# Optimization experiments

Hardware: AMD Instinct MI355X
Metric: run time of the kernel (lower is better)

The kernel has to match this reference:

```python
import jax, jax.numpy as jnp
import numpy as np

B, N, ATTR = 8, 16384, 14
G, M = 256, 32
ENC = 1024
DIM, DEPTH, HEADS = 384, 12, 6
HID = 4 * DIM
FETCH = (3, 7, 11)


def setup_inputs() -> dict:
    key = jax.random.key(0)
    ks = iter(jax.random.split(key, 40))
    def rn(shape, s=0.02):
        return jax.random.normal(next(ks), shape, dtype=jnp.float32) * s
    inp = {}
    inp["xyz"] = jax.random.normal(next(ks), (B, N, ATTR), dtype=jnp.float32)
    # T-Net: 6 -> 64 -> 512 -> 36 (6x6 transform)
    inp["tn_c1_w"] = rn((64, 6));    inp["tn_c1_b"] = jnp.zeros((64,), jnp.float32)
    inp["tn_bn1_g"] = jnp.ones((64,), jnp.float32);  inp["tn_bn1_b"] = jnp.zeros((64,), jnp.float32)
    inp["tn_c2_w"] = rn((512, 64));  inp["tn_c2_b"] = jnp.zeros((512,), jnp.float32)
    inp["tn_bn2_g"] = jnp.ones((512,), jnp.float32); inp["tn_bn2_b"] = jnp.zeros((512,), jnp.float32)
    inp["tn_fc_w"] = rn((36, 512));  inp["tn_fc_b"] = jnp.zeros((36,), jnp.float32)
    # PointNet encoder: ATTR -> 128 -> 256 -> 512 -> ENC (1x1 convs)
    for i, (o, c) in enumerate([(128, ATTR), (256, 128), (512, 256), (ENC, 512)], 1):
        inp[f"e_c{i}_w"] = rn((o, c)); inp[f"e_c{i}_b"] = jnp.zeros((o,), jnp.float32)
        inp[f"e_bn{i}_g"] = jnp.ones((o,), jnp.float32); inp[f"e_bn{i}_b"] = jnp.zeros((o,), jnp.float32)
    inp["reduce_w"] = rn((DIM, ENC)); inp["reduce_b"] = jnp.zeros((DIM,), jnp.float32)
    inp["pos1_w"] = rn((128, 3));     inp["pos1_b"] = jnp.zeros((128,), jnp.float32)
    inp["pos2_w"] = rn((DIM, 128));   inp["pos2_b"] = jnp.zeros((DIM,), jnp.float32)
    # transformer blocks, stacked over depth
    inp["ln1_g"] = jnp.ones((DEPTH, DIM), jnp.float32); inp["ln1_b"] = jnp.zeros((DEPTH, DIM), jnp.float32)
    inp["qkv_w"] = rn((DEPTH, 3 * DIM, DIM))
    inp["proj_w"] = rn((DEPTH, DIM, DIM)); inp["proj_b"] = jnp.zeros((DEPTH, DIM), jnp.float32)
    inp["ln2_g"] = jnp.ones((DEPTH, DIM), jnp.float32); inp["ln2_b"] = jnp.zeros((DEPTH, DIM), jnp.float32)
    inp["fc1_w"] = rn((DEPTH, HID, DIM)); inp["fc1_b"] = jnp.zeros((DEPTH, HID), jnp.float32)
    inp["fc2_w"] = rn((DEPTH, DIM, HID)); inp["fc2_b"] = jnp.zeros((DEPTH, DIM), jnp.float32)
    return inp


def _bn(x, g, b, eps=1e-5):
    # training-mode BatchNorm1d over [batch, length, channel]
    m = jnp.mean(x, axis=(0, 1))
    v = jnp.var(x, axis=(0, 1))
    return (x - m) * jax.lax.rsqrt(v + eps) * g + b


def _lnorm(x, g, b, eps=1e-5):
    m = jnp.mean(x, axis=-1, keepdims=True)
    v = jnp.var(x, axis=-1, keepdims=True)
    return (x - m) * jax.lax.rsqrt(v + eps) * g + b


def _fps(xyz, npoint):
    # sequential farthest point sampling (deterministic start at index 0)
    b, n, _ = xyz.shape
    coords = xyz[:, :, :3]
    bidx = jnp.arange(b)
    def step(carry, _):
        dist, far = carry
        c = coords[bidx, far]                                   # [B,3]
        d = jnp.sum((coords - c[:, None, :]) ** 2, axis=-1)     # [B,N]
        dist = jnp.minimum(dist, d)
        return (dist, jnp.argmax(dist, axis=-1)), far
    init = (jnp.full((b, n), 1e10, jnp.float32), jnp.zeros((b,), jnp.int32))
    _, idxs = jax.lax.scan(step, init, None, length=npoint)
    return jnp.transpose(idxs)                                   # [B,npoint]


def _forward(xyz, tn_c1_w, tn_c1_b, tn_bn1_g, tn_bn1_b, tn_c2_w, tn_c2_b, tn_bn2_g, tn_bn2_b,
             tn_fc_w, tn_fc_b,
             e_c1_w, e_c1_b, e_bn1_g, e_bn1_b, e_c2_w, e_c2_b, e_bn2_g, e_bn2_b,
             e_c3_w, e_c3_b, e_bn3_g, e_bn3_b, e_c4_w, e_c4_b, e_bn4_g, e_bn4_b,
             reduce_w, reduce_b, pos1_w, pos1_b, pos2_w, pos2_b,
             ln1_g, ln1_b, qkv_w, proj_w, proj_b, ln2_g, ln2_b,
             fc1_w, fc1_b, fc2_w, fc2_b):
    b = xyz.shape[0]
    # ---- grouping: FPS + attribute-space KNN (cdist over all A attrs) ----
    cidx = _fps(xyz, G)                                          # [B,G]
    cattrs = jnp.take_along_axis(xyz, cidx[:, :, None], axis=1)  # [B,G,A]
    center = cattrs[:, :, :3]                                    # [B,G,3]
    d2 = (jnp.sum(cattrs ** 2, -1)[:, :, None] + jnp.sum(xyz ** 2, -1)[:, None, :]
          - 2.0 * jnp.einsum('bga,bna->bgn', cattrs, xyz))       # [B,G,N]
    _, knn = jax.lax.top_k(-d2, M)                               # [B,G,M] smallest dists
    nb = jnp.take_along_axis(xyz, knn.reshape(b, G * M)[:, :, None], axis=1)
    nb = nb.reshape(b, G, M, ATTR)
    nb = jnp.concatenate([nb[..., :3] - center[:, :, None, :], nb[..., 3:]], axis=-1)
    # ---- PointNet encoder with 6x6 T-Net on the first 6 attributes ----
    pg = nb.reshape(b * G, M, ATTR)
    x6 = pg[:, :, :6]
    h = jax.nn.relu(_bn(jnp.einsum('bmc,oc->bmo', x6, tn_c1_w) + tn_c1_b, tn_bn1_g, tn_bn1_b))
    h = jax.nn.relu(_bn(jnp.einsum('bmc,oc->bmo', h, tn_c2_w) + tn_c2_b, tn_bn2_g, tn_bn2_b))
    h = jnp.max(h, axis=1)                                       # [BG,512]
    t = (h @ tn_fc_w.T + tn_fc_b + jnp.eye(6, dtype=jnp.float32).reshape(36)).reshape(-1, 6, 6)
    pg = jnp.concatenate([jnp.einsum('bmc,bck->bmk', x6, t), pg[:, :, 6:]], axis=-1)
    p = jax.nn.relu(_bn(jnp.einsum('bmc,oc->bmo', pg, e_c1_w) + e_c1_b, e_bn1_g, e_bn1_b))
    p = jax.nn.relu(_bn(jnp.einsum('bmc,oc->bmo', p, e_c2_w) + e_c2_b, e_bn2_g, e_bn2_b))
    p = jax.nn.relu(_bn(jnp.einsum('bmc,oc->bmo', p, e_c3_w) + e_c3_b, e_bn3_g, e_bn3_b))
    p = _bn(jnp.einsum('bmc,oc->bmo', p, e_c4_w) + e_c4_b, e_bn4_g, e_bn4_b)
    tokens = jnp.max(p, axis=1).reshape(b, G, ENC)               # [B,G,ENC]
    # ---- transformer over group tokens, pos added each layer ----
    x = tokens @ reduce_w.T + reduce_b                           # [B,G,DIM]
    pos = jax.nn.gelu(center @ pos1_w.T + pos1_b) @ pos2_w.T + pos2_b
    scale = (DIM // HEADS) ** -0.5
    feats = []
    for i in range(DEPTH):
        h_in = x + pos
        y = _lnorm(h_in, ln1_g[i], ln1_b[i])
        qkv = jnp.einsum('bnc,oc->bno', y, qkv_w[i]).reshape(b, G, 3, HEADS, DIM // HEADS)
        q, k, v = jnp.moveaxis(qkv, 2, 0)                        # each [B,G,H,D]
        a = jax.nn.softmax(jnp.einsum('bnhd,bmhd->bhnm', q, k) * scale, axis=-1)
        o = jnp.einsum('bhnm,bmhd->bnhd', a, v).reshape(b, G, DIM)
        x = h_in + (jnp.einsum('bnc,oc->bno', o, proj_w[i]) + proj_b[i])
        y = _lnorm(x, ln2_g[i], ln2_b[i])
        y = jax.nn.gelu(jnp.einsum('bnc,oc->bno', y, fc1_w[i]) + fc1_b[i])
        x = x + (jnp.einsum('bnc,oc->bno', y, fc2_w[i]) + fc2_b[i])
        if i in FETCH:
            feats.append(x)
    return jnp.stack(feats)                                      # [3,B,G,DIM]


def reference(xyz, tn_c1_w, tn_c1_b, tn_bn1_g, tn_bn1_b, tn_c2_w, tn_c2_b, tn_bn2_g, tn_bn2_b,
              tn_fc_w, tn_fc_b,
              e_c1_w, e_c1_b, e_bn1_g, e_bn1_b, e_c2_w, e_c2_b, e_bn2_g, e_bn2_b,
              e_c3_w, e_c3_b, e_bn3_g, e_bn3_b, e_c4_w, e_c4_b, e_bn4_g, e_bn4_b,
              reduce_w, reduce_b, pos1_w, pos1_b, pos2_w, pos2_b,
              ln1_g, ln1_b, qkv_w, proj_w, proj_b, ln2_g, ln2_b,
              fc1_w, fc1_b, fc2_w, fc2_b):
    return _forward(xyz, tn_c1_w, tn_c1_b, tn_bn1_g, tn_bn1_b, tn_c2_w, tn_c2_b, tn_bn2_g, tn_bn2_b,
                    tn_fc_w, tn_fc_b,
                    e_c1_w, e_c1_b, e_bn1_g, e_bn1_b, e_c2_w, e_c2_b, e_bn2_g, e_bn2_b,
                    e_c3_w, e_c3_b, e_bn3_g, e_bn3_b, e_c4_w, e_c4_b, e_bn4_g, e_bn4_b,
                    reduce_w, reduce_b, pos1_w, pos1_b, pos2_w, pos2_b,
                    ln1_g, ln1_b, qkv_w, proj_w, proj_b, ln2_g, ln2_b,
                    fc1_w, fc1_b, fc2_w, fc2_b)
```

## Files before the change

kernel.cpp:

```cpp
#include <hip/hip_runtime.h>
#include <hip/hip_bf16.h>
#include <math.h>

typedef __hip_bfloat16 bf16;
typedef __attribute__((ext_vector_type(8))) short bfrag;
typedef __attribute__((ext_vector_type(4))) float f32x4;

constexpr int B_ = 8, N_ = 16384, ATTR_ = 14, G_ = 256, M_ = 32;
constexpr int BG = B_ * G_;
constexpr int ROWS = BG * M_;
constexpr int DIM_ = 384, HEADS_ = 6;

static inline int cdiv(int a, int b) { return (a + b - 1) / b; }

__device__ __forceinline__ float gelu_f(float x) {
  float x3 = x * x * x;
  float t = tanhf(0.7978845608028654f * (x + 0.044715f * x3));
  return 0.5f * x * (1.0f + t);
}

__global__ __launch_bounds__(1024) void fps_kernel(const float* __restrict__ xyz,
                                                   int* __restrict__ cidx) {
  const int b = blockIdx.x;
  const int tid = threadIdx.x;
  const float* base = xyz + (size_t)b * N_ * ATTR_;
  float px[16], py[16], pz[16], dist[16];
#pragma unroll
  for (int j = 0; j < 16; ++j) {
    int n = tid + j * 1024;
    px[j] = base[(size_t)n * ATTR_ + 0];
    py[j] = base[(size_t)n * ATTR_ + 1];
    pz[j] = base[(size_t)n * ATTR_ + 2];
    dist[j] = 1e10f;
  }
  __shared__ float s_v[16];
  __shared__ int s_i[16];
  __shared__ float s_cx, s_cy, s_cz;
  int far = 0;
  float cx = base[0], cy = base[1], cz = base[2];
  for (int g = 0; g < G_; ++g) {
    if (tid == 0) cidx[b * G_ + g] = far;
    float best = -1.0f; int bi = 0;
#pragma unroll
    for (int j = 0; j < 16; ++j) {
      float dx = __fsub_rn(px[j], cx);
      float dy = __fsub_rn(py[j], cy);
      float dz = __fsub_rn(pz[j], cz);
      float d = __fadd_rn(__fadd_rn(__fmul_rn(dx, dx), __fmul_rn(dy, dy)), __fmul_rn(dz, dz));
      float nd = fminf(dist[j], d);
      dist[j] = nd;
      int n = tid + j * 1024;
      if (nd > best) { best = nd; bi = n; }
    }
#pragma unroll
    for (int off = 32; off > 0; off >>= 1) {
      float ov = __shfl_down(best, off);
      int   oi = __shfl_down(bi, off);
      if (ov > best || (ov == best && oi < bi)) { best = ov; bi = oi; }
    }
    if ((tid & 63) == 0) { s_v[tid >> 6] = best; s_i[tid >> 6] = bi; }
    __syncthreads();
    float bv = s_v[0]; int win = s_i[0];
#pragma unroll
    for (int w = 1; w < 16; ++w) {
      float v = s_v[w]; int iw = s_i[w];
      if (v > bv || (v == bv && iw < win)) { bv = v; win = iw; }
    }
    if (tid == (win & 1023)) {
      int jw = win >> 10;
      float wx = px[0], wy = py[0], wz = pz[0];
#pragma unroll
      for (int j = 1; j < 16; ++j)
        if (j == jw) { wx = px[j]; wy = py[j]; wz = pz[j]; }
      s_cx = wx; s_cy = wy; s_cz = wz;
    }
    __syncthreads();
    far = win; cx = s_cx; cy = s_cy; cz = s_cz;
  }
}

__global__ void pn2_kernel(const float* __restrict__ xyz, float* __restrict__ pn2) {
  int gid = blockIdx.x * blockDim.x + threadIdx.x;
  if (gid >= B_ * N_) return;
  const float* p = xyz + (size_t)gid * ATTR_;
  float s = 0.f;
#pragma unroll
  for (int a = 0; a < ATTR_; ++a) s = __fadd_rn(s, __fmul_rn(p[a], p[a]));
  pn2[gid] = s;
}

__global__ __launch_bounds__(256) void knn_kernel(const float* __restrict__ xyz,
                                                  const float* __restrict__ pn2,
                                                  const int* __restrict__ cidx,
                                                  int* __restrict__ knn) {
  const int bg = blockIdx.x;
  const int b = bg >> 8;
  const int tid = threadIdx.x;
  const int wave = tid >> 6, lane = tid & 63;
  __shared__ float d2s[N_];
  __shared__ float catt[ATTR_];
  __shared__ float wv[4][32];
  __shared__ int wi[4][32];
  const float* xb = xyz + (size_t)b * N_ * ATTR_;
  if (tid == 0) {
    int ci = cidx[bg];
    for (int a = 0; a < ATTR_; ++a) catt[a] = xb[(size_t)ci * ATTR_ + a];
  }
  __syncthreads();
  float cn2 = 0.f;
#pragma unroll
  for (int a = 0; a < ATTR_; ++a) cn2 = __fadd_rn(cn2, __fmul_rn(catt[a], catt[a]));
  const float* pnb = pn2 + (size_t)b * N_;
  const int base = tid * 64;
  float bv = 3.0e38f; int bi = 0;
  for (int j = 0; j < 64; ++j) {
    int n = base + j;
    const float* p = xb + (size_t)n * ATTR_;
    float dot = 0.f;
#pragma unroll
    for (int a = 0; a < ATTR_; ++a) dot = __fadd_rn(dot, __fmul_rn(catt[a], p[a]));
    float v = __fsub_rn(__fadd_rn(cn2, pnb[n]), __fmul_rn(2.0f, dot));
    d2s[n] = v;
    if (v < bv) { bv = v; bi = n; }
  }
  for (int m = 0; m < M_; ++m) {
    float v = bv; int i = bi;
#pragma unroll
    for (int off = 1; off < 64; off <<= 1) {
      float ov = __shfl_xor(v, off);
      int   oi = __shfl_xor(i, off);
      if (ov < v || (ov == v && oi < i)) { v = ov; i = oi; }
    }
    if (lane == 0) { wv[wave][m] = v; wi[wave][m] = i; }
    if (i >= base && i < base + 64) {
      d2s[i] = 3.0e38f;
      bv = 3.0e38f; bi = base;
#pragma unroll 4
      for (int jj = 0; jj < 16; ++jj) {
        float4 q4 = *(const float4*)(d2s + base + jj * 4);
        int n0 = base + jj * 4;
        if (q4.x < bv) { bv = q4.x; bi = n0; }
        if (q4.y < bv) { bv = q4.y; bi = n0 + 1; }
        if (q4.z < bv) { bv = q4.z; bi = n0 + 2; }
        if (q4.w < bv) { bv = q4.w; bi = n0 + 3; }
      }
    }
  }
  __syncthreads();
  if (tid == 0) {
    int h0 = 0, h1 = 0, h2 = 0, h3 = 0;
    for (int m = 0; m < M_; ++m) {
      float mv = 3.0e38f; int midx = 0x7fffffff; int mw = 0;
      if (h0 < 32) { float v = wv[0][h0]; int ix = wi[0][h0]; if (v < mv || (v == mv && ix < midx)) { mv = v; midx = ix; mw = 0; } }
      if (h1 < 32) { float v = wv[1][h1]; int ix = wi[1][h1]; if (v < mv || (v == mv && ix < midx)) { mv = v; midx = ix; mw = 1; } }
      if (h2 < 32) { float v = wv[2][h2]; int ix = wi[2][h2]; if (v < mv || (v == mv && ix < midx)) { mv = v; midx = ix; mw = 2; } }
      if (h3 < 32) { float v = wv[3][h3]; int ix = wi[3][h3]; if (v < mv || (v == mv && ix < midx)) { mv = v; midx = ix; mw = 3; } }
      knn[(size_t)bg * M_ + m] = midx;
      if (mw == 0) ++h0; else if (mw == 1) ++h1; else if (mw == 2) ++h2; else ++h3;
    }
  }
}

__global__ void pg_build_kernel(const float* __restrict__ xyz, const int* __restrict__ cidx,
                                const int* __restrict__ knn, float* __restrict__ pg,
                                float* __restrict__ center) {
  int gid = blockIdx.x * blockDim.x + threadIdx.x;
  if (gid >= ROWS) return;
  int bg = gid >> 5, mm = gid & 31;
  int b = bg >> 8;
  int ci = cidx[bg];
  int ni = knn[(size_t)bg * M_ + mm];
  const float* c = xyz + ((size_t)b * N_ + ci) * ATTR_;
  const float* p = xyz + ((size_t)b * N_ + ni) * ATTR_;
  float* o = pg + (size_t)gid * ATTR_;
#pragma unroll
  for (int a = 0; a < 3; ++a) o[a] = __fsub_rn(p[a], c[a]);
#pragma unroll
  for (int a = 3; a < ATTR_; ++a) o[a] = p[a];
  if (mm == 0) {
    center[bg * 3 + 0] = c[0]; center[bg * 3 + 1] = c[1]; center[bg * 3 + 2] = c[2];
  }
}

template<bool ABF, bool BIAS, bool GELUE, bool EYE, bool OBF>
__global__ __launch_bounds__(256) void gemm_kernel(
    const void* __restrict__ Ap, const float* __restrict__ W,
    const float* __restrict__ bias, void* __restrict__ Cp,
    int Mrows, int K, int OC, int lda) {
  __shared__ float As[16][68];
  __shared__ float Ws[16][68];
  const int tid = threadIdx.x;
  const int tx = tid & 15, ty = tid >> 4;
  const int row0 = blockIdx.y * 64, col0 = blockIdx.x * 64;
  float acc[4][4] = {{0.f}};
  const float* Af = (const float*)Ap;
  const bf16* Ab = (const bf16*)Ap;
  const int r = tid >> 2;
  const int kb = (tid & 3) * 4;
  for (int k0 = 0; k0 < K; k0 += 16) {
#pragma unroll
    for (int i = 0; i < 4; ++i) {
      int kk = kb + i, kg = k0 + kk;
      float a = 0.f, w = 0.f;
      if (kg < K) {
        size_t ai = (size_t)(row0 + r) * lda + kg;
        a = ABF ? __bfloat162float(Ab[ai]) : Af[ai];
        int oc = col0 + r;
        if (oc < OC) w = W[(size_t)oc * K + kg];
      }
      As[kk][r] = a;
      Ws[kk][r] = w;
    }
    __syncthreads();
#pragma unroll
    for (int kk = 0; kk < 16; ++kk) {
      float av[4], bv[4];
#pragma unroll
      for (int i = 0; i < 4; ++i) av[i] = As[kk][ty * 4 + i];
#pragma unroll
      for (int j = 0; j < 4; ++j) bv[j] = Ws[kk][tx * 4 + j];
#pragma unroll
      for (int i = 0; i < 4; ++i)
#pragma unroll
        for (int j = 0; j < 4; ++j) acc[i][j] = fmaf(av[i], bv[j], acc[i][j]);
    }
    __syncthreads();
  }
#pragma unroll
  for (int i = 0; i < 4; ++i) {
    int row = row0 + ty * 4 + i;
#pragma unroll
    for (int j = 0; j < 4; ++j) {
      int c = col0 + tx * 4 + j;
      if (c >= OC) continue;
      float v = acc[i][j];
      if (BIAS) v += bias[c];
      if (EYE) { if ((c / 6) == (c % 6)) v += 1.0f; }
      if (GELUE) v = gelu_f(v);
      size_t oi = (size_t)row * OC + c;
      if (OBF) ((bf16*)Cp)[oi] = __float2bfloat16(v);
      else ((float*)Cp)[oi] = v;
    }
  }
}

template<int BM, int BN, bool WF32, bool BIAS, bool GELUE, bool RES, bool OBF>
__global__ __launch_bounds__(256) void mfma_gemm(
    const bf16* __restrict__ A, const void* __restrict__ Wp,
    const float* __restrict__ bias, const float* __restrict__ res,
    void* __restrict__ Cp, int K, int OC) {
  constexpr int MR = BM / 32;
  constexpr int NR = BN / 32;
  __shared__ __align__(16) bf16 As[BM * 64];
  __shared__ __align__(16) bf16 Ws[BN * 64];
  const int tid = threadIdx.x;
  const int wid = tid >> 6, lane = tid & 63;
  const int wm = wid >> 1, wn = wid & 1;
  const int l15 = lane & 15, l4 = lane >> 4;
  const int row0 = blockIdx.y * BM, col0 = blockIdx.x * BN;
  const float* Wf = (const float*)Wp;
  const bf16* Wb = (const bf16*)Wp;
  f32x4 acc[MR][NR];
#pragma unroll
  for (int m = 0; m < MR; ++m)
#pragma unroll
    for (int n = 0; n < NR; ++n) acc[m][n] = (f32x4){0.f, 0.f, 0.f, 0.f};

  for (int k0 = 0; k0 < K; k0 += 64) {
#pragma unroll
    for (int t = tid; t < BM * 8; t += 256) {
      int r = t >> 3, c = t & 7;
      uint4 v = *(const uint4*)(A + (size_t)(row0 + r) * K + k0 + c * 8);
      *(uint4*)(As + r * 64 + ((c ^ (r & 7)) * 8)) = v;
    }
#pragma unroll
    for (int t = tid; t < BN * 8; t += 256) {
      int r = t >> 3, c = t & 7;
      uint4 v;
      if (WF32) {
        const float* src = Wf + (size_t)(col0 + r) * K + k0 + c * 8;
        float4 f0 = *(const float4*)src;
        float4 f1 = *(const float4*)(src + 4);
        bf16 tmp[8];
        tmp[0] = __float2bfloat16(f0.x); tmp[1] = __float2bfloat16(f0.y);
        tmp[2] = __float2bfloat16(f0.z); tmp[3] = __float2bfloat16(f0.w);
        tmp[4] = __float2bfloat16(f1.x); tmp[5] = __float2bfloat16(f1.y);
        tmp[6] = __float2bfloat16(f1.z); tmp[7] = __float2bfloat16(f1.w);
        v = *(uint4*)tmp;
      } else {
        v = *(const uint4*)(Wb + (size_t)(col0 + r) * K + k0 + c * 8);
      }
      *(uint4*)(Ws + r * 64 + ((c ^ (r & 7)) * 8)) = v;
    }
    __syncthreads();
#pragma unroll
    for (int kk = 0; kk < 2; ++kk) {
      const int chunk = kk * 4 + l4;
      bfrag a[MR], b[NR];
#pragma unroll
      for (int m = 0; m < MR; ++m) {
        int R = wm * (BM / 2) + m * 16 + l15;
        a[m] = *(const bfrag*)(As + R * 64 + ((chunk ^ (R & 7)) * 8));
      }
#pragma unroll
      for (int n = 0; n < NR; ++n) {
        int R = wn * (BN / 2) + n * 16 + l15;
        b[n] = *(const bfrag*)(Ws + R * 64 + ((chunk ^ (R & 7)) * 8));
      }
#pragma unroll
      for (int m = 0; m < MR; ++m)
#pragma unroll
        for (int n = 0; n < NR; ++n)
          acc[m][n] = __builtin_amdgcn_mfma_f32_16x16x32_bf16(a[m], b[n], acc[m][n], 0, 0, 0);
    }
    __syncthreads();
  }
#pragma unroll
  for (int m = 0; m < MR; ++m) {
    int rbase = row0 + wm * (BM / 2) + m * 16 + l4 * 4;
#pragma unroll
    for (int n = 0; n < NR; ++n) {
      int c = col0 + wn * (BN / 2) + n * 16 + l15;
      float bs = BIAS ? bias[c] : 0.f;
#pragma unroll
      for (int j = 0; j < 4; ++j) {
        int row = rbase + j;
        float v = acc[m][n][j] + bs;
        if (GELUE) v = gelu_f(v);
        if (RES) v += res[(size_t)row * OC + c];
        size_t oi = (size_t)row * OC + c;
        if (OBF) ((bf16*)Cp)[oi] = __float2bfloat16(v);
        else ((float*)Cp)[oi] = v;
      }
    }
  }
}

__global__ __launch_bounds__(256) void bn_stats_kernel(const bf16* __restrict__ Y,
                                                       float* __restrict__ stats, int C) {
  const int r0 = blockIdx.x * 256;
  const int tid = threadIdx.x;
  for (int c = tid; c < C; c += 256) {
    float s = 0.f, q = 0.f;
    for (int r = 0; r < 256; ++r) {
      float y = __bfloat162float(Y[(size_t)(r0 + r) * C + c]);
      s += y; q += y * y;
    }
    atomicAdd(&stats[c], s);
    atomicAdd(&stats[C + c], q);
  }
}

__global__ void bn_fin_kernel(const float* __restrict__ stats, const float* __restrict__ g,
                              const float* __restrict__ b, float* __restrict__ ss, int C) {
  int c = blockIdx.x * blockDim.x + threadIdx.x;
  if (c >= C) return;
  const float inv_n = 1.0f / (float)ROWS;
  float m = stats[c] * inv_n;
  float v = stats[C + c] * inv_n - m * m;
  float sc = g[c] * (1.0f / sqrtf(v + 1e-5f));
  ss[c] = sc;
  ss[C + c] = b[c] - m * sc;
}

__global__ __launch_bounds__(256) void bnrelu_kernel(bf16* __restrict__ Y,
                                                     const float* __restrict__ ss,
                                                     int C, int total8) {
  for (int i = blockIdx.x * blockDim.x + threadIdx.x; i < total8; i += gridDim.x * blockDim.x) {
    size_t base = (size_t)i * 8;
    int c0 = (int)(base % (size_t)C);
    uint4 v = *(uint4*)(Y + base);
    bf16* e = (bf16*)&v;
#pragma unroll
    for (int j = 0; j < 8; ++j) {
      float f = fmaf(__bfloat162float(e[j]), ss[c0 + j], ss[C + c0 + j]);
      e[j] = __float2bfloat16(fmaxf(f, 0.f));
    }
    *(uint4*)(Y + base) = v;
  }
}

template<bool RELU, bool OBF>
__global__ void maxpool_kernel(const bf16* __restrict__ Y, const float* __restrict__ ss,
                               void* __restrict__ out, int C) {
  int gid = blockIdx.x * blockDim.x + threadIdx.x;
  if (gid >= BG * C) return;
  int bg = gid / C, c = gid - bg * C;
  float sc = ss[c], sh = ss[C + c];
  float m = -3.0e38f;
  for (int j = 0; j < M_; ++j) {
    float y = __bfloat162float(Y[((size_t)bg * M_ + j) * C + c]);
    float v = fmaf(y, sc, sh);
    if (RELU) v = fmaxf(v, 0.f);
    m = fmaxf(m, v);
  }
  if (OBF) ((bf16*)out)[gid] = __float2bfloat16(m);
  else ((float*)out)[gid] = m;
}

__global__ void tnet_apply_kernel(const float* __restrict__ pg, const float* __restrict__ tmat,
                                  float* __restrict__ pg2) {
  int row = blockIdx.x * blockDim.x + threadIdx.x;
  if (row >= ROWS) return;
  int bg = row >> 5;
  const float* t = tmat + (size_t)bg * 36;
  const float* in = pg + (size_t)row * ATTR_;
  float* o = pg2 + (size_t)row * ATTR_;
  float x[6];
#pragma unroll
  for (int c = 0; c < 6; ++c) x[c] = in[c];
#pragma unroll
  for (int k = 0; k < 6; ++k) {
    float s = 0.f;
#pragma unroll
    for (int c = 0; c < 6; ++c) s = fmaf(x[c], t[c * 6 + k], s);
    o[k] = s;
  }
#pragma unroll
  for (int a = 6; a < ATTR_; ++a) o[a] = in[a];
}

template<bool ADDPOS>
__global__ __launch_bounds__(128) void ln_kernel(const float* __restrict__ x,
                                                 const float* __restrict__ pos,
                                                 const float* __restrict__ g,
                                                 const float* __restrict__ b,
                                                 float* __restrict__ hin,
                                                 bf16* __restrict__ y) {
  const int row = blockIdx.x;
  const int tid = threadIdx.x;
  float v[3];
  float s = 0.f;
#pragma unroll
  for (int i = 0; i < 3; ++i) {
    int c = tid + i * 128;
    float t = x[(size_t)row * DIM_ + c];
    if (ADDPOS) t += pos[(size_t)row * DIM_ + c];
    v[i] = t; s += t;
  }
  for (int off = 32; off > 0; off >>= 1) s += __shfl_down(s, off);
  __shared__ float sa[2], sb[2];
  if ((tid & 63) == 0) sa[tid >> 6] = s;
  __syncthreads();
  float mean = (sa[0] + sa[1]) * (1.0f / DIM_);
  float q = 0.f;
#pragma unroll
  for (int i = 0; i < 3; ++i) { float d = v[i] - mean; q += d * d; }
  for (int off = 32; off > 0; off >>= 1) q += __shfl_down(q, off);
  if ((tid & 63) == 0) sb[tid >> 6] = q;
  __syncthreads();
  float var = (sb[0] + sb[1]) * (1.0f / DIM_);
  float rs = 1.0f / sqrtf(var + 1e-5f);
#pragma unroll
  for (int i = 0; i < 3; ++i) {
    int c = tid + i * 128;
    if (ADDPOS) hin[(size_t)row * DIM_ + c] = v[i];
    y[(size_t)row * DIM_ + c] = __float2bfloat16(fmaf((v[i] - mean) * rs, g[c], b[c]));
  }
}

__global__ __launch_bounds__(256) void attn_kernel(const float* __restrict__ qkv,
                                                   bf16* __restrict__ obuf) {
  const int blk = blockIdx.x;
  const int qt = blk & 3;
  const int bh = blk >> 2;
  const int b = bh / HEADS_, h = bh % HEADS_;
  const int tid = threadIdx.x;
  __shared__ float Qs[64][65];
  __shared__ float KVs[256][65];
  __shared__ float Ss[64][257];
  const int n0 = qt * 64;
  const size_t qbase = (size_t)b * G_ * (3 * DIM_);
#pragma unroll 4
  for (int i = 0; i < 16; ++i) {
    int idx = i * 256 + tid;
    int qr = idx >> 6, d = idx & 63;
    Qs[qr][d] = qkv[qbase + (size_t)(n0 + qr) * (3 * DIM_) + h * 64 + d];
  }
#pragma unroll 4
  for (int i = 0; i < 64; ++i) {
    int idx = i * 256 + tid;
    int kr = idx >> 6, d = idx & 63;
    KVs[kr][d] = qkv[qbase + (size_t)kr * (3 * DIM_) + DIM_ + h * 64 + d];
  }
  __syncthreads();
  const int q = tid >> 2, kl = tid & 3;
  float lmax = -3.0e38f;
#pragma unroll 4
  for (int kk = 0; kk < 64; ++kk) {
    int k = kl + kk * 4;
    float s = 0.f;
#pragma unroll
    for (int d = 0; d < 64; ++d) s = fmaf(Qs[q][d], KVs[k][d], s);
    s *= 0.125f;
    Ss[q][k] = s;
    lmax = fmaxf(lmax, s);
  }
  lmax = fmaxf(lmax, __shfl_xor(lmax, 1));
  lmax = fmaxf(lmax, __shfl_xor(lmax, 2));
  float lsum = 0.f;
#pragma unroll 4
  for (int kk = 0; kk < 64; ++kk) {
    int k = kl + kk * 4;
    float e = expf(Ss[q][k] - lmax);
    Ss[q][k] = e;
    lsum += e;
  }
  lsum += __shfl_xor(lsum, 1);
  lsum += __shfl_xor(lsum, 2);
#pragma unroll 4
  for (int kk = 0; kk < 64; ++kk) {
    int k = kl + kk * 4;
    Ss[q][k] = Ss[q][k] / lsum;
  }
  __syncthreads();
#pragma unroll 4
  for (int i = 0; i < 64; ++i) {
    int idx = i * 256 + tid;
    int kr = idx >> 6, d = idx & 63;
    KVs[kr][d] = qkv[qbase + (size_t)kr * (3 * DIM_) + 2 * DIM_ + h * 64 + d];
  }
  __syncthreads();
  float oacc[16];
#pragma unroll
  for (int i = 0; i < 16; ++i) oacc[i] = 0.f;
  for (int k = 0; k < 256; ++k) {
    float s = Ss[q][k];
#pragma unroll
    for (int dd = 0; dd < 16; ++dd) oacc[dd] = fmaf(s, KVs[k][kl + dd * 4], oacc[dd]);
  }
  bf16* ob = obuf + (size_t)(b * G_ + n0 + q) * DIM_ + h * 64;
#pragma unroll
  for (int dd = 0; dd < 16; ++dd) ob[kl + dd * 4] = __float2bfloat16(oacc[dd]);
}

extern "C" void kernel_launch(void* const* d_in, const int* in_sizes, int n_in,
                              void* d_out, int out_size, void* d_ws, size_t ws_size,
                              hipStream_t stream) {
  const float* xyz      = (const float*)d_in[0];
  const float* tn_c1_w  = (const float*)d_in[1];
  const float* tn_c1_b  = (const float*)d_in[2];
  const float* tn_bn1_g = (const float*)d_in[3];
  const float* tn_bn1_b = (const float*)d_in[4];
  const float* tn_c2_w  = (const float*)d_in[5];
  const float* tn_c2_b  = (const float*)d_in[6];
  const float* tn_bn2_g = (const float*)d_in[7];
  const float* tn_bn2_b = (const float*)d_in[8];
  const float* tn_fc_w  = (const float*)d_in[9];
  const float* tn_fc_b  = (const float*)d_in[10];
  const float* e_c1_w = (const float*)d_in[11];
  const float* e_c1_b = (const float*)d_in[12];
  const float* e_bn1_g = (const float*)d_in[13];
  const float* e_bn1_b = (const float*)d_in[14];
  const float* e_c2_w = (const float*)d_in[15];
  const float* e_c2_b = (const float*)d_in[16];
  const float* e_bn2_g = (const float*)d_in[17];
  const float* e_bn2_b = (const float*)d_in[18];
  const float* e_c3_w = (const float*)d_in[19];
  const float* e_c3_b = (const float*)d_in[20];
  const float* e_bn3_g = (const float*)d_in[21];
  const float* e_bn3_b = (const float*)d_in[22];
  const float* e_c4_w = (const float*)d_in[23];
  const float* e_c4_b = (const float*)d_in[24];
  const float* e_bn4_g = (const float*)d_in[25];
  const float* e_bn4_b = (const float*)d_in[26];
  const float* reduce_w = (const float*)d_in[27];
  const float* reduce_b = (const float*)d_in[28];
  const float* pos1_w = (const float*)d_in[29];
  const float* pos1_b = (const float*)d_in[30];
  const float* pos2_w = (const float*)d_in[31];
  const float* pos2_b = (const float*)d_in[32];
  const float* ln1_g = (const float*)d_in[33];
  const float* ln1_b = (const float*)d_in[34];
  const float* qkv_w = (const float*)d_in[35];
  const float* proj_w = (const float*)d_in[36];
  const float* proj_b = (const float*)d_in[37];
  const float* ln2_g = (const float*)d_in[38];
  const float* ln2_b = (const float*)d_in[39];
  const float* fc1_w = (const float*)d_in[40];
  const float* fc1_b = (const float*)d_in[41];
  const float* fc2_w = (const float*)d_in[42];
  const float* fc2_b = (const float*)d_in[43];
  (void)in_sizes; (void)n_in; (void)out_size; (void)ws_size;

  char* ws = (char*)d_ws;
  size_t off = 0;
  auto alloc = [&](size_t bytes) -> void* {
    void* p = ws + off;
    off = (off + bytes + 255) & ~(size_t)255;
    return p;
  };

  char* stats_begin = ws + off;
  float* stats_tn1 = (float*)alloc(2 * 64 * 4);
  float* stats_tn2 = (float*)alloc(2 * 512 * 4);
  float* stats_e1 = (float*)alloc(2 * 128 * 4);
  float* stats_e2 = (float*)alloc(2 * 256 * 4);
  float* stats_e3 = (float*)alloc(2 * 512 * 4);
  float* stats_e4 = (float*)alloc(2 * 1024 * 4);
  size_t stats_len = (size_t)((ws + off) - stats_begin);
  float* ss_tn1 = (float*)alloc(2 * 64 * 4);
  float* ss_tn2 = (float*)alloc(2 * 512 * 4);
  float* ss_e1 = (float*)alloc(2 * 128 * 4);
  float* ss_e2 = (float*)alloc(2 * 256 * 4);
  float* ss_e3 = (float*)alloc(2 * 512 * 4);
  float* ss_e4 = (float*)alloc(2 * 1024 * 4);
  int* cidx = (int*)alloc((size_t)BG * 4);
  int* knn = (int*)alloc((size_t)ROWS * 4);
  float* pn2 = (float*)alloc((size_t)B_ * N_ * 4);
  float* center = (float*)alloc((size_t)BG * 3 * 4);
  float* pg = (float*)alloc((size_t)ROWS * ATTR_ * 4);
  float* pg2 = (float*)alloc((size_t)ROWS * ATTR_ * 4);
  float* hmax = (float*)alloc((size_t)BG * 512 * 4);
  float* tmat = (float*)alloc((size_t)BG * 36 * 4);
  bf16* tokens = (bf16*)alloc((size_t)BG * 1024 * 2);
  float* xb = (float*)alloc((size_t)BG * DIM_ * 4);
  float* posb = (float*)alloc((size_t)BG * DIM_ * 4);
  float* hinb = (float*)alloc((size_t)BG * DIM_ * 4);
  bf16* yb = (bf16*)alloc((size_t)BG * DIM_ * 2);
  float* qkvb = (float*)alloc((size_t)BG * 3 * DIM_ * 4);
  bf16* obf = (bf16*)alloc((size_t)BG * DIM_ * 2);
  bf16* hmlp = (bf16*)alloc((size_t)BG * 1536 * 2);
  float* p1 = (float*)alloc((size_t)BG * 128 * 4);
  bf16* Bbuf0 = (bf16*)alloc((size_t)ROWS * 512 * 2);
  bf16* Bbuf1 = (bf16*)alloc((size_t)ROWS * 1024 * 2);

  hipMemsetAsync(stats_begin, 0, stats_len, stream);

  fps_kernel<<<B_, 1024, 0, stream>>>(xyz, cidx);
  pn2_kernel<<<cdiv(B_ * N_, 256), 256, 0, stream>>>(xyz, pn2);
  knn_kernel<<<BG, 256, 0, stream>>>(xyz, pn2, cidx, knn);
  pg_build_kernel<<<cdiv(ROWS, 256), 256, 0, stream>>>(xyz, cidx, knn, pg, center);

  gemm_kernel<false, true, false, false, true>
      <<<dim3(1, ROWS / 64), 256, 0, stream>>>(pg, tn_c1_w, tn_c1_b, Bbuf0, ROWS, 6, 64, ATTR_);
  bn_stats_kernel<<<ROWS / 256, 256, 0, stream>>>(Bbuf0, stats_tn1, 64);
  bn_fin_kernel<<<1, 64, 0, stream>>>(stats_tn1, tn_bn1_g, tn_bn1_b, ss_tn1, 64);
  bnrelu_kernel<<<2048, 256, 0, stream>>>(Bbuf0, ss_tn1, 64, ROWS * 64 / 8);
  mfma_gemm<128, 128, true, true, false, false, true>
      <<<dim3(4, ROWS / 128), 256, 0, stream>>>(Bbuf0, tn_c2_w, tn_c2_b, nullptr, Bbuf1, 64, 512);
  bn_stats_kernel<<<ROWS / 256, 256, 0, stream>>>(Bbuf1, stats_tn2, 512);
  bn_fin_kernel<<<2, 256, 0, stream>>>(stats_tn2, tn_bn2_g, tn_bn2_b, ss_tn2, 512);
  maxpool_kernel<true, false><<<cdiv(BG * 512, 256), 256, 0, stream>>>(Bbuf1, ss_tn2, hmax, 512);
  gemm_kernel<false, true, false, true, false>
      <<<dim3(1, BG / 64), 256, 0, stream>>>(hmax, tn_fc_w, tn_fc_b, tmat, BG, 512, 36, 512);
  tnet_apply_kernel<<<cdiv(ROWS, 256), 256, 0, stream>>>(pg, tmat, pg2);

  gemm_kernel<false, true, false, false, true>
      <<<dim3(2, ROWS / 64), 256, 0, stream>>>(pg2, e_c1_w, e_c1_b, Bbuf0, ROWS, ATTR_, 128, ATTR_);
  bn_stats_kernel<<<ROWS / 256, 256, 0, stream>>>(Bbuf0, stats_e1, 128);
  bn_fin_kernel<<<1, 128, 0, stream>>>(stats_e1, e_bn1_g, e_bn1_b, ss_e1, 128);
  bnrelu_kernel<<<2048, 256, 0, stream>>>(Bbuf0, ss_e1, 128, ROWS * 128 / 8);
  mfma_gemm<128, 128, true, true, false, false, true>
      <<<dim3(2, ROWS / 128), 256, 0, stream>>>(Bbuf0, e_c2_w, e_c2_b, nullptr, Bbuf1, 128, 256);
  bn_stats_kernel<<<ROWS / 256, 256, 0, stream>>>(Bbuf1, stats_e2, 256);
  bn_fin_kernel<<<1, 256, 0, stream>>>(stats_e2, e_bn2_g, e_bn2_b, ss_e2, 256);
  bnrelu_kernel<<<2048, 256, 0, stream>>>(Bbuf1, ss_e2, 256, ROWS * 256 / 8);
  mfma_gemm<128, 128, true, true, false, false, true>
      <<<dim3(4, ROWS / 128), 256, 0, stream>>>(Bbuf1, e_c3_w, e_c3_b, nullptr, Bbuf0, 256, 512);
  bn_stats_kernel<<<ROWS / 256, 256, 0, stream>>>(Bbuf0, stats_e3, 512);
  bn_fin_kernel<<<2, 256, 0, stream>>>(stats_e3, e_bn3_g, e_bn3_b, ss_e3, 512);
  bnrelu_kernel<<<2048, 256, 0, stream>>>(Bbuf0, ss_e3, 512, ROWS * 512 / 8);
  mfma_gemm<128, 128, true, true, false, false, true>
      <<<dim3(8, ROWS / 128), 256, 0, stream>>>(Bbuf0, e_c4_w, e_c4_b, nullptr, Bbuf1, 512, 1024);
  bn_stats_kernel<<<ROWS / 256, 256, 0, stream>>>(Bbuf1, stats_e4, 1024);
  bn_fin_kernel<<<4, 256, 0, stream>>>(stats_e4, e_bn4_g, e_bn4_b, ss_e4, 1024);
  maxpool_kernel<false, true><<<cdiv(BG * 1024, 256), 256, 0, stream>>>(Bbuf1, ss_e4, tokens, 1024);

  mfma_gemm<64, 64, true, true, false, false, false>
      <<<dim3(6, BG / 64), 256, 0, stream>>>(tokens, reduce_w, reduce_b, nullptr, xb, 1024, DIM_);
  gemm_kernel<false, true, true, false, false>
      <<<dim3(2, BG / 64), 256, 0, stream>>>(center, pos1_w, pos1_b, p1, BG, 3, 128, 3);
  gemm_kernel<false, true, false, false, false>
      <<<dim3(6, BG / 64), 256, 0, stream>>>(p1, pos2_w, pos2_b, posb, BG, 128, DIM_, 128);

  int slot = 0;
  for (int i = 0; i < 12; ++i) {
    ln_kernel<true><<<BG, 128, 0, stream>>>(xb, posb, ln1_g + (size_t)i * DIM_,
                                            ln1_b + (size_t)i * DIM_, hinb, yb);
    mfma_gemm<64, 128, true, false, false, false, false>
        <<<dim3(9, BG / 64), 256, 0, stream>>>(yb, qkv_w + (size_t)i * 3 * DIM_ * DIM_,
                                               nullptr, nullptr, qkvb, DIM_, 3 * DIM_);
    attn_kernel<<<B_ * HEADS_ * 4, 256, 0, stream>>>(qkvb, obf);
    mfma_gemm<64, 64, true, true, false, true, false>
        <<<dim3(6, BG / 64), 256, 0, stream>>>(obf, proj_w + (size_t)i * DIM_ * DIM_,
                                               proj_b + (size_t)i * DIM_, hinb, xb, DIM_, DIM_);
    ln_kernel<false><<<BG, 128, 0, stream>>>(xb, nullptr, ln2_g + (size_t)i * DIM_,
                                             ln2_b + (size_t)i * DIM_, nullptr, yb);
    mfma_gemm<64, 128, true, true, true, false, true>
        <<<dim3(12, BG / 64), 256, 0, stream>>>(yb, fc1_w + (size_t)i * 1536 * DIM_,
                                                fc1_b + (size_t)i * 1536, nullptr, hmlp,
                                                DIM_, 1536);
    mfma_gemm<64, 64, true, true, false, true, false>
        <<<dim3(6, BG / 64), 256, 0, stream>>>(hmlp, fc2_w + (size_t)i * DIM_ * 1536,
                                               fc2_b + (size_t)i * DIM_, xb, xb, 1536, DIM_);
    if (i == 3 || i == 7 || i == 11) {
      hipMemcpyAsync((float*)d_out + (size_t)slot * BG * DIM_, xb,
                     (size_t)BG * DIM_ * 4, hipMemcpyDeviceToDevice, stream);
      ++slot;
    }
  }
}
```

Baseline: 4.791 ms.

## Fuse LayerNorm into full-row GEMM epilogues and use DPP wave reductions

Adds a GEMM kernel that computes a full 384-wide output row per block, so LayerNorm statistics can be reduced in the epilogue. It replaces the separate ln_kernel launches after the reduce, proj and fc2 GEMMs, with fc2 also producing the next block's LN1 input. The pos MLP second layer moves to the MFMA GEMM with a bf16 intermediate, and the FPS/kNN wave argmax/argmin use DPP row ops instead of shuffles. The trade-off is that only BG/64 = 32 blocks launch for the fused GEMMs, which is low occupancy on a large GPU. Variance is computed as E[x²]−mean², which is less numerically robust than the old two-pass form.

```diff
diff --git a/kernel.cpp b/kernel.cpp
--- a/kernel.cpp
+++ b/kernel.cpp
@@ -17,6 +17,32 @@
   float x3 = x * x * x;
   float t = tanhf(0.7978845608028654f * (x + 0.044715f * x3));
   return 0.5f * x * (1.0f + t);
+}
+
+#define DPP_STEP_MAX(CTRL)                                                              \
+  {                                                                                     \
+    int ovi = __builtin_amdgcn_update_dpp(__float_as_int(v), __float_as_int(v),         \
+                                          CTRL, 0xf, 0xf, false);                       \
+    int oii = __builtin_amdgcn_update_dpp(i, i, CTRL, 0xf, 0xf, false);                 \
+    float ov = __int_as_float(ovi);                                                     \
+    if (ov > v || (ov == v && oii < i)) { v = ov; i = oii; }                            \
+  }
+#define DPP_STEP_MIN(CTRL)                                                              \
+  {                                                                                     \
+    int ovi = __builtin_amdgcn_update_dpp(__float_as_int(v), __float_as_int(v),         \
+                                          CTRL, 0xf, 0xf, false);                       \
+    int oii = __builtin_amdgcn_update_dpp(i, i, CTRL, 0xf, 0xf, false);                 \
+    float ov = __int_as_float(ovi);                                                     \
+    if (ov < v || (ov == v && oii < i)) { v = ov; i = oii; }                            \
+  }
+
+__device__ __forceinline__ void wave_argmax_dpp(float& v, int& i) {
+  DPP_STEP_MAX(0x111) DPP_STEP_MAX(0x112) DPP_STEP_MAX(0x114) DPP_STEP_MAX(0x118)
+  DPP_STEP_MAX(0x142) DPP_STEP_MAX(0x143)
+}
+__device__ __forceinline__ void wave_argmin_dpp(float& v, int& i) {
+  DPP_STEP_MIN(0x111) DPP_STEP_MIN(0x112) DPP_STEP_MIN(0x114) DPP_STEP_MIN(0x118)
+  DPP_STEP_MIN(0x142) DPP_STEP_MIN(0x143)
 }
 
 __global__ __launch_bounds__(1024) void fps_kernel(const float* __restrict__ xyz,
@@ -40,7 +66,7 @@
   float cx = base[0], cy = base[1], cz = base[2];
   for (int g = 0; g < G_; ++g) {
     if (tid == 0) cidx[b * G_ + g] = far;
-    float best = -1.0f; int bi = 0;
+    float v = -1.0f; int i = 0;
 #pragma unroll
     for (int j = 0; j < 16; ++j) {
       float dx = __fsub_rn(px[j], cx);
@@ -50,21 +76,16 @@
       float nd = fminf(dist[j], d);
       dist[j] = nd;
       int n = tid + j * 1024;
-      if (nd > best) { best = nd; bi = n; }
-    }
-#pragma unroll
-    for (int off = 32; off > 0; off >>= 1) {
-      float ov = __shfl_down(best, off);
-      int   oi = __shfl_down(bi, off);
-      if (ov > best || (ov == best && oi < bi)) { best = ov; bi = oi; }
-    }
-    if ((tid & 63) == 0) { s_v[tid >> 6] = best; s_i[tid >> 6] = bi; }
+      if (nd > v) { v = nd; i = n; }
+    }
+    wave_argmax_dpp(v, i);
+    if ((tid & 63) == 63) { s_v[tid >> 6] = v; s_i[tid >> 6] = i; }
     __syncthreads();
     float bv = s_v[0]; int win = s_i[0];
 #pragma unroll
     for (int w = 1; w < 16; ++w) {
-      float v = s_v[w]; int iw = s_i[w];
-      if (v > bv || (v == bv && iw < win)) { bv = v; win = iw; }
+      float vv = s_v[w]; int iw = s_i[w];
+      if (vv > bv || (vv == bv && iw < win)) { bv = vv; win = iw; }
     }
     if (tid == (win & 1023)) {
       int jw = win >> 10;
@@ -125,15 +146,11 @@
   }
   for (int m = 0; m < M_; ++m) {
     float v = bv; int i = bi;
-#pragma unroll
-    for (int off = 1; off < 64; off <<= 1) {
-      float ov = __shfl_xor(v, off);
-      int   oi = __shfl_xor(i, off);
-      if (ov < v || (ov == v && oi < i)) { v = ov; i = oi; }
-    }
-    if (lane == 0) { wv[wave][m] = v; wi[wave][m] = i; }
-    if (i >= base && i < base + 64) {
-      d2s[i] = 3.0e38f;
+    wave_argmin_dpp(v, i);
+    int win = __builtin_amdgcn_readlane(i, 63);
+    if (lane == 63) { wv[wave][m] = v; wi[wave][m] = i; }
+    if (win >= base && win < base + 64) {
+      d2s[win] = 3.0e38f;
       bv = 3.0e38f; bi = base;
 #pragma unroll 4
       for (int jj = 0; jj < 16; ++jj) {
@@ -336,6 +353,151 @@
   }
 }
 
+template<bool RESIN, bool ADDPOS>
+__global__ __launch_bounds__(256) void mfma_gemm_ln(
+    const bf16* __restrict__ A, const float* __restrict__ Wf,
+    const float* __restrict__ bias, const float* __restrict__ res,
+    const float* __restrict__ pos, const float* __restrict__ g,
+    const float* __restrict__ bta, float* __restrict__ xout,
+    float* __restrict__ hout, bf16* __restrict__ yout, int K) {
+  constexpr int BM = 64, BN = 384;
+  constexpr int MR = 2, NR = 12;
+  __shared__ __align__(16) bf16 As[BM * 64];
+  __shared__ __align__(16) bf16 Ws[BN * 64];
+  const int tid = threadIdx.x;
+  const int wid = tid >> 6, lane = tid & 63;
+  const int wm = wid >> 1, wn = wid & 1;
+  const int l15 = lane & 15, l4 = lane >> 4;
+  const int row0 = blockIdx.x * BM;
+  f32x4 acc[MR][NR];
+#pragma unroll
+  for (int m = 0; m < MR; ++m)
+#pragma unroll
+    for (int n = 0; n < NR; ++n) acc[m][n] = (f32x4){0.f, 0.f, 0.f, 0.f};
+
+  for (int k0 = 0; k0 < K; k0 += 64) {
+#pragma unroll
+    for (int t = tid; t < BM * 8; t += 256) {
+      int r = t >> 3, c = t & 7;
+      uint4 v = *(const uint4*)(A + (size_t)(row0 + r) * K + k0 + c * 8);
+      *(uint4*)(As + r * 64 + ((c ^ (r & 7)) * 8)) = v;
+    }
+#pragma unroll
+    for (int t = tid; t < BN * 8; t += 256) {
+      int r = t >> 3, c = t & 7;
+      const float* src = Wf + (size_t)r * K + k0 + c * 8;
+      float4 f0 = *(const float4*)src;
+      float4 f1 = *(const float4*)(src + 4);
+      bf16 tmp[8];
+      tmp[0] = __float2bfloat16(f0.x); tmp[1] = __float2bfloat16(f0.y);
+      tmp[2] = __float2bfloat16(f0.z); tmp[3] = __float2bfloat16(f0.w);
+      tmp[4] = __float2bfloat16(f1.x); tmp[5] = __float2bfloat16(f1.y);
+      tmp[6] = __float2bfloat16(f1.z); tmp[7] = __float2bfloat16(f1.w);
+      uint4 v = *(uint4*)tmp;
+      *(uint4*)(Ws + r * 64 + ((c ^ (r & 7)) * 8)) = v;
+    }
+    __syncthreads();
+#pragma unroll
+    for (int kk = 0; kk < 2; ++kk) {
+      const int chunk = kk * 4 + l4;
+      bfrag a[MR], b[NR];
+#pragma unroll
+      for (int m = 0; m < MR; ++m) {
+        int R = wm * 32 + m * 16 + l15;
+        a[m] = *(const bfrag*)(As + R * 64 + ((chunk ^ (R & 7)) * 8));
+      }
+#pragma unroll
+      for (int n = 0; n < NR; ++n) {
+        int R = wn * 192 + n * 16 + l15;
+        b[n] = *(const bfrag*)(Ws + R * 64 + ((chunk ^ (R & 7)) * 8));
+      }
+#pragma unroll
+      for (int m = 0; m < MR; ++m)
+#pragma unroll
+        for (int n = 0; n < NR; ++n)
+          acc[m][n] = __builtin_amdgcn_mfma_f32_16x16x32_bf16(a[m], b[n], acc[m][n], 0, 0, 0);
+    }
+    __syncthreads();
+  }
+  float s[MR][4], q[MR][4];
+#pragma unroll
+  for (int m = 0; m < MR; ++m)
+#pragma unroll
+    for (int j = 0; j < 4; ++j) { s[m][j] = 0.f; q[m][j] = 0.f; }
+#pragma unroll
+  for (int m = 0; m < MR; ++m) {
+#pragma unroll
+    for (int n = 0; n < NR; ++n) {
+      int c = wn * 192 + n * 16 + l15;
+      float bs = bias[c];
+#pragma unroll
+      for (int j = 0; j < 4; ++j) {
+        int row = row0 + wm * 32 + m * 16 + l4 * 4 + j;
+        float v = acc[m][n][j] + bs;
+        if (RESIN) v += res[(size_t)row * 384 + c];
+        xout[(size_t)row * 384 + c] = v;
+        float h = v;
+        if (ADDPOS) {
+          h += pos[(size_t)row * 384 + c];
+          hout[(size_t)row * 384 + c] = h;
+        }
+        acc[m][n][j] = h;
+        s[m][j] += h;
+        q[m][j] = fmaf(h, h, q[m][j]);
+      }
+    }
+  }
+#pragma unroll
+  for (int off = 1; off < 16; off <<= 1) {
+#pragma unroll
+    for (int m = 0; m < MR; ++m)
+#pragma unroll
+      for (int j = 0; j < 4; ++j) {
+        s[m][j] += __shfl_xor(s[m][j], off);
+        q[m][j] += __shfl_xor(q[m][j], off);
+      }
+  }
+  float* red = (float*)As;
+  if (l15 == 0) {
+#pragma unroll
+    for (int m = 0; m < MR; ++m)
+#pragma unroll
+      for (int j = 0; j < 4; ++j) {
+        int rl = wm * 32 + m * 16 + l4 * 4 + j;
+        red[rl * 2 + wn] = s[m][j];
+        red[128 + rl * 2 + wn] = q[m][j];
+      }
+  }
+  __syncthreads();
+  float mu[MR][4], rs[MR][4];
+#pragma unroll
+  for (int m = 0; m < MR; ++m)
+#pragma unroll
+    for (int j = 0; j < 4; ++j) {
+      int rl = wm * 32 + m * 16 + l4 * 4 + j;
+      float S = red[rl * 2 + 0] + red[rl * 2 + 1];
+      float Q = red[128 + rl * 2 + 0] + red[128 + rl * 2 + 1];
+      float mean = S * (1.0f / 384.0f);
+      float var = Q * (1.0f / 384.0f) - mean * mean;
+      mu[m][j] = mean;
+      rs[m][j] = 1.0f / sqrtf(var + 1e-5f);
+    }
+#pragma unroll
+  for (int m = 0; m < MR; ++m) {
+#pragma unroll
+    for (int n = 0; n < NR; ++n) {
+      int c = wn * 192 + n * 16 + l15;
+      float gc = g[c], bc = bta[c];
+#pragma unroll
+      for (int j = 0; j < 4; ++j) {
+        int row = row0 + wm * 32 + m * 16 + l4 * 4 + j;
+        float y = fmaf((acc[m][n][j] - mu[m][j]) * rs[m][j], gc, bc);
+        yout[(size_t)row * 384 + c] = __float2bfloat16(y);
+      }
+    }
+  }
+}
+
 __global__ __launch_bounds__(256) void bn_stats_kernel(const bf16* __restrict__ Y,
                                                        float* __restrict__ stats, int C) {
   const int r0 = blockIdx.x * 256;
@@ -418,45 +580,6 @@
   }
 #pragma unroll
   for (int a = 6; a < ATTR_; ++a) o[a] = in[a];
-}
-
-template<bool ADDPOS>
-__global__ __launch_bounds__(128) void ln_kernel(const float* __restrict__ x,
-                                                 const float* __restrict__ pos,
-                                                 const float* __restrict__ g,
-                                                 const float* __restrict__ b,
-                                                 float* __restrict__ hin,
-                                                 bf16* __restrict__ y) {
-  const int row = blockIdx.x;
-  const int tid = threadIdx.x;
-  float v[3];
-  float s = 0.f;
-#pragma unroll
-  for (int i = 0; i < 3; ++i) {
-    int c = tid + i * 128;
-    float t = x[(size_t)row * DIM_ + c];
-    if (ADDPOS) t += pos[(size_t)row * DIM_ + c];
-    v[i] = t; s += t;
-  }
-  for (int off = 32; off > 0; off >>= 1) s += __shfl_down(s, off);
-  __shared__ float sa[2], sb[2];
-  if ((tid & 63) == 0) sa[tid >> 6] = s;
-  __syncthreads();
-  float mean = (sa[0] + sa[1]) * (1.0f / DIM_);
-  float q = 0.f;
-#pragma unroll
-  for (int i = 0; i < 3; ++i) { float d = v[i] - mean; q += d * d; }
-  for (int off = 32; off > 0; off >>= 1) q += __shfl_down(q, off);
-  if ((tid & 63) == 0) sb[tid >> 6] = q;
-  __syncthreads();
-  float var = (sb[0] + sb[1]) * (1.0f / DIM_);
-  float rs = 1.0f / sqrtf(var + 1e-5f);
-#pragma unroll
-  for (int i = 0; i < 3; ++i) {
-    int c = tid + i * 128;
-    if (ADDPOS) hin[(size_t)row * DIM_ + c] = v[i];
-    y[(size_t)row * DIM_ + c] = __float2bfloat16(fmaf((v[i] - mean) * rs, g[c], b[c]));
-  }
 }
 
 __global__ __launch_bounds__(256) void attn_kernel(const float* __restrict__ qkv,
@@ -621,7 +744,7 @@
   float* qkvb = (float*)alloc((size_t)BG * 3 * DIM_ * 4);
   bf16* obf = (bf16*)alloc((size_t)BG * DIM_ * 2);
   bf16* hmlp = (bf16*)alloc((size_t)BG * 1536 * 2);
-  float* p1 = (float*)alloc((size_t)BG * 128 * 4);
+  bf16* p1b = (bf16*)alloc((size_t)BG * 128 * 2);
   bf16* Bbuf0 = (bf16*)alloc((size_t)ROWS * 512 * 2);
   bf16* Bbuf1 = (bf16*)alloc((size_t)ROWS * 1024 * 2);
 
@@ -667,33 +790,35 @@
   bn_fin_kernel<<<4, 256, 0, stream>>>(stats_e4, e_bn4_g, e_bn4_b, ss_e4, 1024);
   maxpool_kernel<false, true><<<cdiv(BG * 1024, 256), 256, 0, stream>>>(Bbuf1, ss_e4, tokens, 1024);
 
-  mfma_gemm<64, 64, true, true, false, false, false>
-      <<<dim3(6, BG / 64), 256, 0, stream>>>(tokens, reduce_w, reduce_b, nullptr, xb, 1024, DIM_);
-  gemm_kernel<false, true, true, false, false>
-      <<<dim3(2, BG / 64), 256, 0, stream>>>(center, pos1_w, pos1_b, p1, BG, 3, 128, 3);
-  gemm_kernel<false, true, false, false, false>
-      <<<dim3(6, BG / 64), 256, 0, stream>>>(p1, pos2_w, pos2_b, posb, BG, 128, DIM_, 128);
+  gemm_kernel<false, true, true, false, true>
+      <<<dim3(2, BG / 64), 256, 0, stream>>>(center, pos1_w, pos1_b, p1b, BG, 3, 128, 3);
+  mfma_gemm<64, 128, true, true, false, false, false>
+      <<<dim3(3, BG / 64), 256, 0, stream>>>(p1b, pos2_w, pos2_b, nullptr, posb, 128, DIM_);
+  mfma_gemm_ln<false, true>
+      <<<BG / 64, 256, 0, stream>>>(tokens, reduce_w, reduce_b, nullptr, posb,
+                                    ln1_g, ln1_b, xb, hinb, yb, 1024);
 
   int slot = 0;
   for (int i = 0; i < 12; ++i) {
-    ln_kernel<true><<<BG, 128, 0, stream>>>(xb, posb, ln1_g + (size_t)i * DIM_,
-                                            ln1_b + (size_t)i * DIM_, hinb, yb);
     mfma_gemm<64, 128, true, false, false, false, false>
         <<<dim3(9, BG / 64), 256, 0, stream>>>(yb, qkv_w + (size_t)i * 3 * DIM_ * DIM_,
                                                nullptr, nullptr, qkvb, DIM_, 3 * DIM_);
     attn_kernel<<<B_ * HEADS_ * 4, 256, 0, stream>>>(qkvb, obf);
-    mfma_gemm<64, 64, true, true, false, true, false>
-        <<<dim3(6, BG / 64), 256, 0, stream>>>(obf, proj_w + (size_t)i * DIM_ * DIM_,
-                                               proj_b + (size_t)i * DIM_, hinb, xb, DIM_, DIM_);
-    ln_kernel<false><<<BG, 128, 0, stream>>>(xb, nullptr, ln2_g + (size_t)i * DIM_,
-                                             ln2_b + (size_t)i * DIM_, nullptr, yb);
+    mfma_gemm_ln<true, false>
+        <<<BG / 64, 256, 0, stream>>>(obf, proj_w + (size_t)i * DIM_ * DIM_,
+                                      proj_b + (size_t)i * DIM_, hinb, nullptr,
+                                      ln2_g + (size_t)i * DIM_, ln2_b + (size_t)i * DIM_,
+                                      xb, nullptr, yb, DIM_);
     mfma_gemm<64, 128, true, true, true, false, true>
         <<<dim3(12, BG / 64), 256, 0, stream>>>(yb, fc1_w + (size_t)i * 1536 * DIM_,
                                                 fc1_b + (size_t)i * 1536, nullptr, hmlp,
                                                 DIM_, 1536);
-    mfma_gemm<64, 64, true, true, false, true, false>
-        <<<dim3(6, BG / 64), 256, 0, stream>>>(hmlp, fc2_w + (size_t)i * DIM_ * 1536,
-                                               fc2_b + (size_t)i * DIM_, xb, xb, 1536, DIM_);
+    int nx = (i < 11) ? i + 1 : 11;
+    mfma_gemm_ln<true, true>
+        <<<BG / 64, 256, 0, stream>>>(hmlp, fc2_w + (size_t)i * DIM_ * 1536,
+                                      fc2_b + (size_t)i * DIM_, xb, posb,
+                                      ln1_g + (size_t)nx * DIM_, ln1_b + (size_t)nx * DIM_,
+                                      xb, hinb, yb, 1536);
     if (i == 3 || i == 7 || i == 11) {
       hipMemcpyAsync((float*)d_out + (size_t)slot * BG * DIM_, xb,
                      (size_t)BG * DIM_ * 4, hipMemcpyDeviceToDevice, stream);
```

Measured after the change: 6.779 ms. 1.41x slower.
